# Kernel tuning notes

Measured on AMD Instinct MI355X. Metric: run time of the kernel, lower is better.

The kernel has to match this reference:

```python
import jax, jax.numpy as jnp
import numpy as np


def setup_inputs() -> dict:
    key = jax.random.key(0)
    k1, k2, k3 = jax.random.split(key, 3)
    C, N, M = 16, 192, 16
    scale = 1.0 / C ** 2
    x = jax.random.normal(k1, (C, N, N, N), dtype=jnp.float32)
    wr = jax.random.uniform(k2, (4, C, C, M, M, M), minval=-scale, maxval=scale, dtype=jnp.float32)
    wi = jax.random.uniform(k3, (4, C, C, M, M, M), minval=-scale, maxval=scale, dtype=jnp.float32)
    return {"x": x, "wr": wr, "wi": wi, "modes": M}


def _mix(w, xf):
    # w: (Cin, Cout, m, m, m) complex; xf: (Cin, m, m, m) complex -> (Cout, m, m, m)
    return jnp.einsum('ixyz,ioxyz->oxyz', xf, w)


def reference(x, wr, wi, modes):
    m = modes
    spatial = x.shape[1:]
    # Forward real FFT over the 3 spatial axes: (C, N, N, N//2+1) complex
    xf = jnp.fft.rfftn(x, axes=(1, 2, 3))
    w = (wr + 1j * wi).astype(xf.dtype)  # (4, Cin, Cout, m, m, m)
    out_fs = jnp.zeros_like(xf)
    # Four low-frequency corner blocks (standard FNO-3D mode truncation)
    out_fs = out_fs.at[:, :m, :m, :m].set(_mix(w[0], xf[:, :m, :m, :m]))
    out_fs = out_fs.at[:, -m:, :m, :m].set(_mix(w[1], xf[:, -m:, :m, :m]))
    out_fs = out_fs.at[:, :m, -m:, :m].set(_mix(w[2], xf[:, :m, -m:, :m]))
    out_fs = out_fs.at[:, -m:, -m:, :m].set(_mix(w[3], xf[:, -m:, -m:, :m]))
    # Inverse real FFT back to physical space
    return jnp.fft.irfftn(out_fs, s=spatial, axes=(1, 2, 3))
```

## Files before the change

kernel.cpp:

```cpp
#include <hip/hip_runtime.h>
#include <math.h>


#define NN 192
#define NC 16
#define NM 16
#define NK2 32

constexpr float TWOPI  = 6.283185307179586476925286766559f;
constexpr float INV_N3 = 1.0f / (192.0f * 192.0f * 192.0f);

__device__ __forceinline__ void fill_T(float2* T) {
  int t = threadIdx.x;
  if (t < NN) {
    float s, c;
    sincosf((TWOPI / NN) * (float)t, &s, &c);
    T[t] = make_float2(c, s);
  }
}

__global__ __launch_bounds__(256) void k1_fwd_z(const float* __restrict__ x,
                                                float2* __restrict__ A) {
  __shared__ float xs[64 * 193];
  __shared__ float2 T[NN];
  const int t = threadIdx.x;
  fill_T(T);
  const int rowBase = blockIdx.x * 64;
  const float4* src = (const float4*)(x + (size_t)rowBase * NN);
#pragma unroll
  for (int k = 0; k < 12; ++k) {
    int i = t + k * 256;
    float4 v = src[i];
    int fi = i << 2;
    int row = fi / NN;
    int z = fi - row * NN;
    float* d = &xs[row * 193 + z];
    d[0] = v.x; d[1] = v.y; d[2] = v.z; d[3] = v.w;
  }
  __syncthreads();
  const int kz = t & 15;
  const int r0 = (t >> 4) << 2;
  float ar[4] = {0.f, 0.f, 0.f, 0.f};
  float ai[4] = {0.f, 0.f, 0.f, 0.f};
  int p = 0;
#pragma unroll 8
  for (int z = 0; z < NN; ++z) {
    float2 w = T[p];
    p += kz; p = (p >= NN) ? p - NN : p;
#pragma unroll
    for (int r = 0; r < 4; ++r) {
      float xv = xs[(r0 + r) * 193 + z];
      ar[r] = fmaf(xv, w.x, ar[r]);
      ai[r] = fmaf(-xv, w.y, ai[r]);
    }
  }
  float2* dst = A + (size_t)rowBase * NM;
#pragma unroll
  for (int r = 0; r < 4; ++r)
    dst[(r0 + r) * NM + kz] = make_float2(ar[r], ai[r]);
}

__global__ __launch_bounds__(256) void k2_fwd_y(const float2* __restrict__ A,
                                                float2* __restrict__ B) {
  __shared__ __align__(16) float2 As[NN * NM];
  __shared__ float2 T[NN];
  const int t = threadIdx.x;
  fill_T(T);
  const int cx = blockIdx.x;
  const float4* src = (const float4*)(A + (size_t)cx * NN * NM);
  float4* dl = (float4*)As;
#pragma unroll
  for (int k = 0; k < 6; ++k) dl[t + k * 256] = src[t + k * 256];
  __syncthreads();
  const int kz = t & 15;
  const int kyq = t >> 4;
  const int s1 = 176 + kyq;
  float2 a0 = make_float2(0.f, 0.f), a1 = make_float2(0.f, 0.f);
  int p0 = 0, p1 = 0;
#pragma unroll 4
  for (int y = 0; y < NN; ++y) {
    float2 a = As[y * NM + kz];
    float2 w0 = T[p0]; p0 += kyq; p0 = (p0 >= NN) ? p0 - NN : p0;
    float2 w1 = T[p1]; p1 += s1;  p1 = (p1 >= NN) ? p1 - NN : p1;
    a0.x = fmaf(a.x, w0.x, fmaf(a.y, w0.y, a0.x));
    a0.y = fmaf(a.y, w0.x, fmaf(-a.x, w0.y, a0.y));
    a1.x = fmaf(a.x, w1.x, fmaf(a.y, w1.y, a1.x));
    a1.y = fmaf(a.y, w1.x, fmaf(-a.x, w1.y, a1.y));
  }
  float2* dst = B + (size_t)cx * NK2 * NM;
  dst[kyq * NM + kz] = a0;
  dst[(16 + kyq) * NM + kz] = a1;
}

__global__ __launch_bounds__(256) void k3_fwd_x(const float2* __restrict__ B,
                                                float2* __restrict__ Xf) {
  __shared__ __align__(16) float2 Bs[NN * NM];
  __shared__ float2 T[NN];
  const int t = threadIdx.x;
  fill_T(T);
  const int c = blockIdx.x >> 5, ky = blockIdx.x & 31;
#pragma unroll
  for (int k = 0; k < 6; ++k) {
    int i = t + k * 256;
    int xx = i >> 3, q = i & 7;
    ((float4*)Bs)[i] = *((const float4*)(B + ((size_t)(c * NN + xx) * NK2 + ky) * NM) + q);
  }
  __syncthreads();
  const int kz = t & 15, kxq = t >> 4;
  const int s1 = 176 + kxq;
  float2 a0 = make_float2(0.f, 0.f), a1 = make_float2(0.f, 0.f);
  int p0 = 0, p1 = 0;
#pragma unroll 4
  for (int xx = 0; xx < NN; ++xx) {
    float2 b = Bs[xx * NM + kz];
    float2 w0 = T[p0]; p0 += kxq; p0 = (p0 >= NN) ? p0 - NN : p0;
    float2 w1 = T[p1]; p1 += s1;  p1 = (p1 >= NN) ? p1 - NN : p1;
    a0.x = fmaf(b.x, w0.x, fmaf(b.y, w0.y, a0.x));
    a0.y = fmaf(b.y, w0.x, fmaf(-b.x, w0.y, a0.y));
    a1.x = fmaf(b.x, w1.x, fmaf(b.y, w1.y, a1.x));
    a1.y = fmaf(b.y, w1.x, fmaf(-b.x, w1.y, a1.y));
  }
  Xf[((size_t)(c * NK2 + kxq) * NK2 + ky) * NM + kz] = a0;
  Xf[((size_t)(c * NK2 + 16 + kxq) * NK2 + ky) * NM + kz] = a1;
}

__global__ __launch_bounds__(256) void k4_mix(const float2* __restrict__ Xf,
                                              const float* __restrict__ wr,
                                              const float* __restrict__ wi,
                                              float2* __restrict__ Y) {
  const int tm = blockIdx.x * 256 + threadIdx.x;
  const int kz = tm & 15, ky = (tm >> 4) & 31, kx = tm >> 9;
  const int q = (kx >= 16 ? 1 : 0) + (ky >= 16 ? 2 : 0);
  const int modeW = ((kx & 15) * 16 + (ky & 15)) * 16 + kz;
  float xr[NC], xi[NC];
#pragma unroll
  for (int i = 0; i < NC; ++i) {
    float2 v = Xf[i * 16384 + tm];
    xr[i] = v.x; xi[i] = v.y;
  }
  const float scale = (kz == 0 ? 1.0f : 2.0f) * INV_N3;
#pragma unroll 1
  for (int o = 0; o < NC; ++o) {
    float cr = 0.f, ci = 0.f;
#pragma unroll
    for (int i = 0; i < NC; ++i) {
      size_t wIdx = (size_t)((q * 16 + i) * 16 + o) * 4096 + modeW;
      float a = wr[wIdx], b = wi[wIdx];
      cr = fmaf(xr[i], a, fmaf(-xi[i], b, cr));
      ci = fmaf(xr[i], b, fmaf(xi[i], a, ci));
    }
    Y[o * 16384 + tm] = make_float2(cr * scale, ci * scale);
  }
}

__global__ __launch_bounds__(256) void k5_inv_x(const float2* __restrict__ Y,
                                                float2* __restrict__ G1) {
  __shared__ __align__(16) float2 Ys[NK2 * NM];
  __shared__ float2 T[NN];
  const int t = threadIdx.x;
  fill_T(T);
  const int c = blockIdx.x >> 5, ky = blockIdx.x & 31;
  {
    int kx = t >> 3, qq = t & 7;
    ((float4*)Ys)[t] = *((const float4*)(Y + (size_t)c * 16384 + (size_t)kx * (NK2 * NM) + ky * NM) + qq);
  }
  __syncthreads();
  const int kz = t & 15, xq = t >> 4;
#pragma unroll 1
  for (int j = 0; j < 12; ++j) {
    const int xx = xq + 16 * j;
    float2 acc = make_float2(0.f, 0.f);
    const int step = xx;
    int p = 0;
#pragma unroll
    for (int k = 0; k < 16; ++k) {
      float2 v = Ys[k * NM + kz];
      float2 w = T[p]; p += step; p = (p >= NN) ? p - NN : p;
      acc.x = fmaf(v.x, w.x, fmaf(-v.y, w.y, acc.x));
      acc.y = fmaf(v.y, w.x, fmaf( v.x, w.y, acc.y));
    }
    int p2 = (176 * xx) % NN;
#pragma unroll
    for (int k = 0; k < 16; ++k) {
      float2 v = Ys[(16 + k) * NM + kz];
      float2 w = T[p2]; p2 += step; p2 = (p2 >= NN) ? p2 - NN : p2;
      acc.x = fmaf(v.x, w.x, fmaf(-v.y, w.y, acc.x));
      acc.y = fmaf(v.y, w.x, fmaf( v.x, w.y, acc.y));
    }
    G1[((size_t)(c * NN + xx) * NK2 + ky) * NM + kz] = acc;
  }
}

__global__ __launch_bounds__(256) void k6_inv_y(const float2* __restrict__ G1,
                                                float2* __restrict__ G2) {
  __shared__ __align__(16) float2 Gs[NK2 * NM];
  __shared__ float2 T[NN];
  const int t = threadIdx.x;
  fill_T(T);
  const int cx = blockIdx.x;
  ((float4*)Gs)[t] = ((const float4*)(G1 + (size_t)cx * NK2 * NM))[t];
  __syncthreads();
  const int kz = t & 15, yq = t >> 4;
#pragma unroll 1
  for (int j = 0; j < 12; ++j) {
    const int y = yq + 16 * j;
    float2 acc = make_float2(0.f, 0.f);
    const int step = y;
    int p = 0;
#pragma unroll
    for (int k = 0; k < 16; ++k) {
      float2 v = Gs[k * NM + kz];
      float2 w = T[p]; p += step; p = (p >= NN) ? p - NN : p;
      acc.x = fmaf(v.x, w.x, fmaf(-v.y, w.y, acc.x));
      acc.y = fmaf(v.y, w.x, fmaf( v.x, w.y, acc.y));
    }
    int p2 = (176 * y) % NN;
#pragma unroll
    for (int k = 0; k < 16; ++k) {
      float2 v = Gs[(16 + k) * NM + kz];
      float2 w = T[p2]; p2 += step; p2 = (p2 >= NN) ? p2 - NN : p2;
      acc.x = fmaf(v.x, w.x, fmaf(-v.y, w.y, acc.x));
      acc.y = fmaf(v.y, w.x, fmaf( v.x, w.y, acc.y));
    }
    G2[((size_t)cx * NN + y) * NM + kz] = acc;
  }
}

__global__ __launch_bounds__(192) void k7_inv_z(const float2* __restrict__ G2,
                                                float* __restrict__ out) {
  __shared__ __align__(16) float2 Gs[NN * NM];
  __shared__ float2 T[NN];
  const int t = threadIdx.x;
  fill_T(T);
  const int cx = blockIdx.x;
  const float4* src = (const float4*)(G2 + (size_t)cx * NN * NM);
#pragma unroll
  for (int k = 0; k < 8; ++k) ((float4*)Gs)[t + k * 192] = src[t + k * 192];
  __syncthreads();
  const int z = t;
  float twc[16], tws[16];
#pragma unroll
  for (int kz = 0; kz < 16; ++kz) {
    float2 w = T[(kz * z) % NN];
    twc[kz] = w.x; tws[kz] = w.y;
  }
  const float4* Gs4 = (const float4*)Gs;
  float* obase = out + (size_t)cx * NN * NN;
#pragma unroll 2
  for (int y = 0; y < NN; ++y) {
    float acc = 0.f;
#pragma unroll
    for (int h = 0; h < 8; ++h) {
      float4 g = Gs4[y * 8 + h];
      acc = fmaf(g.x, twc[2 * h],     fmaf(-g.y, tws[2 * h],     acc));
      acc = fmaf(g.z, twc[2 * h + 1], fmaf(-g.w, tws[2 * h + 1], acc));
    }
    obase[y * NN + z] = acc;
  }
}

extern "C" void kernel_launch(void* const* d_in, const int* in_sizes, int n_in,
                              void* d_out, int out_size, void* d_ws, size_t ws_size,
                              hipStream_t stream) {
  const float* x  = (const float*)d_in[0];
  const float* wr = (const float*)d_in[1];
  const float* wi = (const float*)d_in[2];
  float* out = (float*)d_out;

  float2* A  = (float2*)d_ws;
  float2* B  = A  + 9437184;
  float2* Xf = B  + 1572864;
  float2* Y  = Xf + 262144;
  float2* G1 = B;
  float2* G2 = A;

  k1_fwd_z<<<dim3(9216), dim3(256), 0, stream>>>(x, A);
  k2_fwd_y<<<dim3(3072), dim3(256), 0, stream>>>(A, B);
  k3_fwd_x<<<dim3(512),  dim3(256), 0, stream>>>(B, Xf);
  k4_mix  <<<dim3(64),   dim3(256), 0, stream>>>(Xf, wr, wi, Y);
  k5_inv_x<<<dim3(512),  dim3(256), 0, stream>>>(Y, G1);
  k6_inv_y<<<dim3(3072), dim3(256), 0, stream>>>(G1, G2);
  k7_inv_z<<<dim3(3072), dim3(192), 0, stream>>>(G2, out);
}
```

Before: 1.121 ms.

## Fuse forward z/y and inverse y/z DFT stages; parallelize mix over output channels

Forward z-DFT and y-DFT now run in one kernel per (c,x) slab, and the z-transformed intermediate stays in shared memory, so the large A buffer is never written or read from global memory. The inverse y and z stages are merged the same way, dropping the G2 round trip. The spectral mix kernel now gives each block a single output channel, going from 64 blocks to 1024 to fill the GPU better, at the cost of reloading Xf once per output channel. The fused kernels use more shared memory and do serial sub-batches, which may lower occupancy.

```diff
diff --git a/kernel.cpp b/kernel.cpp
--- a/kernel.cpp
+++ b/kernel.cpp
@@ -19,61 +19,54 @@
   }
 }
 
-__global__ __launch_bounds__(256) void k1_fwd_z(const float* __restrict__ x,
-                                                float2* __restrict__ A) {
-  __shared__ float xs[64 * 193];
-  __shared__ float2 T[NN];
-  const int t = threadIdx.x;
-  fill_T(T);
-  const int rowBase = blockIdx.x * 64;
-  const float4* src = (const float4*)(x + (size_t)rowBase * NN);
-#pragma unroll
-  for (int k = 0; k < 12; ++k) {
-    int i = t + k * 256;
-    float4 v = src[i];
-    int fi = i << 2;
-    int row = fi / NN;
-    int z = fi - row * NN;
-    float* d = &xs[row * 193 + z];
-    d[0] = v.x; d[1] = v.y; d[2] = v.z; d[3] = v.w;
-  }
-  __syncthreads();
+__global__ __launch_bounds__(256) void k12_fwd_zy(const float* __restrict__ x,
+                                                  float2* __restrict__ B) {
+  __shared__ float xs[48 * 193];
+  __shared__ __align__(16) float2 As[NN * NM];
+  __shared__ float2 T[NN];
+  const int t = threadIdx.x;
+  fill_T(T);
+  const int cx = blockIdx.x;
   const int kz = t & 15;
-  const int r0 = (t >> 4) << 2;
-  float ar[4] = {0.f, 0.f, 0.f, 0.f};
-  float ai[4] = {0.f, 0.f, 0.f, 0.f};
-  int p = 0;
+  const int grp = t >> 4;
+  const int r0 = grp * 3;
+
+#pragma unroll 1
+  for (int b = 0; b < 4; ++b) {
+    const float4* src = (const float4*)(x + ((size_t)cx * NN + b * 48) * NN);
+    __syncthreads();
+#pragma unroll
+    for (int k = 0; k < 9; ++k) {
+      int i = t + k * 256;
+      float4 v = src[i];
+      int fi = i << 2;
+      int row = fi / NN;
+      int z = fi - row * NN;
+      float* d = &xs[row * 193 + z];
+      d[0] = v.x; d[1] = v.y; d[2] = v.z; d[3] = v.w;
+    }
+    __syncthreads();
+    float ar[3] = {0.f, 0.f, 0.f};
+    float ai[3] = {0.f, 0.f, 0.f};
+    int p = 0;
 #pragma unroll 8
-  for (int z = 0; z < NN; ++z) {
-    float2 w = T[p];
-    p += kz; p = (p >= NN) ? p - NN : p;
-#pragma unroll
-    for (int r = 0; r < 4; ++r) {
-      float xv = xs[(r0 + r) * 193 + z];
-      ar[r] = fmaf(xv, w.x, ar[r]);
-      ai[r] = fmaf(-xv, w.y, ai[r]);
-    }
-  }
-  float2* dst = A + (size_t)rowBase * NM;
-#pragma unroll
-  for (int r = 0; r < 4; ++r)
-    dst[(r0 + r) * NM + kz] = make_float2(ar[r], ai[r]);
-}
-
-__global__ __launch_bounds__(256) void k2_fwd_y(const float2* __restrict__ A,
-                                                float2* __restrict__ B) {
-  __shared__ __align__(16) float2 As[NN * NM];
-  __shared__ float2 T[NN];
-  const int t = threadIdx.x;
-  fill_T(T);
-  const int cx = blockIdx.x;
-  const float4* src = (const float4*)(A + (size_t)cx * NN * NM);
-  float4* dl = (float4*)As;
-#pragma unroll
-  for (int k = 0; k < 6; ++k) dl[t + k * 256] = src[t + k * 256];
-  __syncthreads();
-  const int kz = t & 15;
-  const int kyq = t >> 4;
+    for (int z = 0; z < NN; ++z) {
+      float2 w = T[p];
+      p += kz; p = (p >= NN) ? p - NN : p;
+#pragma unroll
+      for (int r = 0; r < 3; ++r) {
+        float xv = xs[(r0 + r) * 193 + z];
+        ar[r] = fmaf(xv, w.x, ar[r]);
+        ai[r] = fmaf(-xv, w.y, ai[r]);
+      }
+    }
+#pragma unroll
+    for (int r = 0; r < 3; ++r)
+      As[(b * 48 + r0 + r) * NM + kz] = make_float2(ar[r], ai[r]);
+  }
+  __syncthreads();
+
+  const int kyq = grp;
   const int s1 = 176 + kyq;
   float2 a0 = make_float2(0.f, 0.f), a1 = make_float2(0.f, 0.f);
   int p0 = 0, p1 = 0;
@@ -128,29 +121,23 @@
                                               const float* __restrict__ wr,
                                               const float* __restrict__ wi,
                                               float2* __restrict__ Y) {
-  const int tm = blockIdx.x * 256 + threadIdx.x;
+  const int o  = blockIdx.x & 15;
+  const int mc = blockIdx.x >> 4;
+  const int tm = mc * 256 + threadIdx.x;
   const int kz = tm & 15, ky = (tm >> 4) & 31, kx = tm >> 9;
   const int q = (kx >= 16 ? 1 : 0) + (ky >= 16 ? 2 : 0);
   const int modeW = ((kx & 15) * 16 + (ky & 15)) * 16 + kz;
-  float xr[NC], xi[NC];
+  float cr = 0.f, ci = 0.f;
 #pragma unroll
   for (int i = 0; i < NC; ++i) {
     float2 v = Xf[i * 16384 + tm];
-    xr[i] = v.x; xi[i] = v.y;
+    size_t wIdx = (size_t)((q * 16 + i) * 16 + o) * 4096 + modeW;
+    float a = wr[wIdx], b = wi[wIdx];
+    cr = fmaf(v.x, a, fmaf(-v.y, b, cr));
+    ci = fmaf(v.x, b, fmaf(v.y, a, ci));
   }
   const float scale = (kz == 0 ? 1.0f : 2.0f) * INV_N3;
-#pragma unroll 1
-  for (int o = 0; o < NC; ++o) {
-    float cr = 0.f, ci = 0.f;
-#pragma unroll
-    for (int i = 0; i < NC; ++i) {
-      size_t wIdx = (size_t)((q * 16 + i) * 16 + o) * 4096 + modeW;
-      float a = wr[wIdx], b = wi[wIdx];
-      cr = fmaf(xr[i], a, fmaf(-xi[i], b, cr));
-      ci = fmaf(xr[i], b, fmaf(xi[i], a, ci));
-    }
-    Y[o * 16384 + tm] = make_float2(cr * scale, ci * scale);
-  }
+  Y[o * 16384 + tm] = make_float2(cr * scale, ci * scale);
 }
 
 __global__ __launch_bounds__(256) void k5_inv_x(const float2* __restrict__ Y,
@@ -191,25 +178,30 @@
   }
 }
 
-__global__ __launch_bounds__(256) void k6_inv_y(const float2* __restrict__ G1,
-                                                float2* __restrict__ G2) {
-  __shared__ __align__(16) float2 Gs[NK2 * NM];
+__global__ __launch_bounds__(192) void k67_inv_yz(const float2* __restrict__ G1,
+                                                  float* __restrict__ out) {
+  __shared__ __align__(16) float2 Gs1[NK2 * NM];
+  __shared__ __align__(16) float2 As2[NN * NM];
   __shared__ float2 T[NN];
   const int t = threadIdx.x;
   fill_T(T);
   const int cx = blockIdx.x;
-  ((float4*)Gs)[t] = ((const float4*)(G1 + (size_t)cx * NK2 * NM))[t];
-  __syncthreads();
+  {
+    const float4* src = (const float4*)(G1 + (size_t)cx * NK2 * NM);
+    for (int i = t; i < 256; i += 192) ((float4*)Gs1)[i] = src[i];
+  }
+  __syncthreads();
+
   const int kz = t & 15, yq = t >> 4;
 #pragma unroll 1
-  for (int j = 0; j < 12; ++j) {
-    const int y = yq + 16 * j;
+  for (int j = 0; j < 16; ++j) {
+    const int y = yq * 16 + j;
     float2 acc = make_float2(0.f, 0.f);
     const int step = y;
     int p = 0;
 #pragma unroll
     for (int k = 0; k < 16; ++k) {
-      float2 v = Gs[k * NM + kz];
+      float2 v = Gs1[k * NM + kz];
       float2 w = T[p]; p += step; p = (p >= NN) ? p - NN : p;
       acc.x = fmaf(v.x, w.x, fmaf(-v.y, w.y, acc.x));
       acc.y = fmaf(v.y, w.x, fmaf( v.x, w.y, acc.y));
@@ -217,34 +209,26 @@
     int p2 = (176 * y) % NN;
 #pragma unroll
     for (int k = 0; k < 16; ++k) {
-      float2 v = Gs[(16 + k) * NM + kz];
+      float2 v = Gs1[(16 + k) * NM + kz];
       float2 w = T[p2]; p2 += step; p2 = (p2 >= NN) ? p2 - NN : p2;
       acc.x = fmaf(v.x, w.x, fmaf(-v.y, w.y, acc.x));
       acc.y = fmaf(v.y, w.x, fmaf( v.x, w.y, acc.y));
     }
-    G2[((size_t)cx * NN + y) * NM + kz] = acc;
-  }
-}
-
-__global__ __launch_bounds__(192) void k7_inv_z(const float2* __restrict__ G2,
-                                                float* __restrict__ out) {
-  __shared__ __align__(16) float2 Gs[NN * NM];
-  __shared__ float2 T[NN];
-  const int t = threadIdx.x;
-  fill_T(T);
-  const int cx = blockIdx.x;
-  const float4* src = (const float4*)(G2 + (size_t)cx * NN * NM);
-#pragma unroll
-  for (int k = 0; k < 8; ++k) ((float4*)Gs)[t + k * 192] = src[t + k * 192];
-  __syncthreads();
+    As2[y * NM + kz] = acc;
+  }
+  __syncthreads();
+
   const int z = t;
   float twc[16], tws[16];
-#pragma unroll
-  for (int kz = 0; kz < 16; ++kz) {
-    float2 w = T[(kz * z) % NN];
-    twc[kz] = w.x; tws[kz] = w.y;
-  }
-  const float4* Gs4 = (const float4*)Gs;
+  {
+    int p = 0;
+#pragma unroll
+    for (int k = 0; k < 16; ++k) {
+      float2 w = T[p]; p += z; p = (p >= NN) ? p - NN : p;
+      twc[k] = w.x; tws[k] = w.y;
+    }
+  }
+  const float4* Gs4 = (const float4*)As2;
   float* obase = out + (size_t)cx * NN * NN;
 #pragma unroll 2
   for (int y = 0; y < NN; ++y) {
@@ -267,18 +251,14 @@
   const float* wi = (const float*)d_in[2];
   float* out = (float*)d_out;
 
-  float2* A  = (float2*)d_ws;
-  float2* B  = A  + 9437184;
+  float2* B  = (float2*)d_ws;
   float2* Xf = B  + 1572864;
   float2* Y  = Xf + 262144;
   float2* G1 = B;
-  float2* G2 = A;
-
-  k1_fwd_z<<<dim3(9216), dim3(256), 0, stream>>>(x, A);
-  k2_fwd_y<<<dim3(3072), dim3(256), 0, stream>>>(A, B);
-  k3_fwd_x<<<dim3(512),  dim3(256), 0, stream>>>(B, Xf);
-  k4_mix  <<<dim3(64),   dim3(256), 0, stream>>>(Xf, wr, wi, Y);
-  k5_inv_x<<<dim3(512),  dim3(256), 0, stream>>>(Y, G1);
-  k6_inv_y<<<dim3(3072), dim3(256), 0, stream>>>(G1, G2);
-  k7_inv_z<<<dim3(3072), dim3(192), 0, stream>>>(G2, out);
-}
+
+  k12_fwd_zy<<<dim3(3072), dim3(256), 0, stream>>>(x, B);
+  k3_fwd_x  <<<dim3(512),  dim3(256), 0, stream>>>(B, Xf);
+  k4_mix    <<<dim3(1024), dim3(256), 0, stream>>>(Xf, wr, wi, Y);
+  k5_inv_x  <<<dim3(512),  dim3(256), 0, stream>>>(Y, G1);
+  k67_inv_yz<<<dim3(3072), dim3(192), 0, stream>>>(G1, out);
+}
```

After: 1.196 ms. +6.6%, slower.
